# Optimization experiments

Measured on AMD Instinct MI355X. Metric: run time of the kernel, lower is better.

## Reference

```python
import jax, jax.numpy as jnp
import numpy as np

B, T, D, H = 8, 4096, 512, 512

def log_g(x):
    # log of g(x) = where(x>=0, x+0.5, sigmoid(x)) computed stably in log space
    return jnp.where(x >= 0, jnp.log(jax.nn.relu(x) + 0.5), -jax.nn.softplus(-x))

def setup_inputs() -> dict:
    key = jax.random.key(0)
    ks = jax.random.split(key, 6)
    x = jax.random.normal(ks[0], (B, T, D), dtype=jnp.float32)
    h0 = jax.random.uniform(ks[1], (B, H), dtype=jnp.float32)
    lim_z = 1.0 / np.sqrt(D)
    Wz = jax.random.uniform(ks[2], (H, D), jnp.float32, -lim_z, lim_z)
    bz = jax.random.uniform(ks[3], (H,), jnp.float32, -lim_z, lim_z)
    Wh = jax.random.uniform(ks[4], (H, D), jnp.float32, -lim_z, lim_z)
    bh = jax.random.uniform(ks[5], (H,), jnp.float32, -lim_z, lim_z)
    return {"x": x, "h0": h0, "Wz": Wz, "bz": bz, "Wh": Wh, "bh": bh}

def reference(x, h0, Wz, bz, Wh, bh):
    # gate pre-activation k: (B,T,H)
    k = jnp.einsum('btd,hd->bth', x, Wz) + bz
    log_z = -jax.nn.softplus(-k)        # log sigmoid(k)
    log_coeffs = -jax.nn.softplus(k)    # log (1 - sigmoid(k))
    log_h0 = log_g(h0)[:, None, :]      # (B,1,H)
    log_tilde_h = log_g(jnp.einsum('btd,hd->bth', x, Wh) + bh)
    # Heinsen log-space parallel scan
    log_values = jnp.concatenate([log_h0, log_z + log_tilde_h], axis=1)  # (B,T+1,H)
    a_star = jnp.pad(jnp.cumsum(log_coeffs, axis=1), ((0, 0), (1, 0), (0, 0)))  # (B,T+1,H)
    log_h = a_star + jax.lax.cumlogsumexp(log_values - a_star, axis=1)
    return jnp.exp(log_h)[:, 1:]  # (B,T,H)
```

## Files before the change

kernel.cpp:

```cpp
#include <hip/hip_runtime.h>
#include <hip/hip_fp16.h>
#include <cstdint>
#include <cstddef>

constexpr int Bb = 8, Tt = 4096, Dd = 512, Hh = 512;
constexpr int Mm = Bb * Tt;
constexpr int CHUNKS = 128;
constexpr int CLEN = Tt / CHUNKS;

typedef short short8 __attribute__((ext_vector_type(8)));
typedef float f32x4 __attribute__((ext_vector_type(4)));

#define BMT 128
#define BHT 128
#define BKT 64

__device__ inline void gload_lds16(const void* g, void* lds) {
  __builtin_amdgcn_global_load_lds(
      (const __attribute__((address_space(1))) unsigned int*)g,
      (__attribute__((address_space(3))) unsigned int*)lds,
      16, 0, 0);
}

__device__ inline unsigned short bf16_rne(float f) {
  unsigned int u = __float_as_uint(f);
  unsigned int r = (u + 0x7FFFu + ((u >> 16) & 1u)) >> 16;
  return (unsigned short)r;
}

__device__ inline uint2 pack4_bf16(const float* p) {
  uint2 hv;
  hv.x = (unsigned)bf16_rne(p[0]) | ((unsigned)bf16_rne(p[1]) << 16);
  hv.y = (unsigned)bf16_rne(p[2]) | ((unsigned)bf16_rne(p[3]) << 16);
  return hv;
}

__global__ __launch_bounds__(256) void prep_all(
    const float* __restrict__ x, const float* __restrict__ Wz,
    const float* __restrict__ Wh, unsigned short* __restrict__ xb,
    unsigned short* __restrict__ Wc) {
  int bid = blockIdx.x;
  if (bid < 16384) {
    size_t i = (size_t)bid * 256 + threadIdx.x;
    float4 w = *(const float4*)(x + i * 4);
    *(uint2*)(xb + i * 4) = pack4_bf16((const float*)&w);
  } else {
    int j = (bid - 16384) * 256 + threadIdx.x;
    const float* src = (j < 65536) ? (Wz + (size_t)j * 4)
                                   : (Wh + (size_t)(j - 65536) * 4);
    float4 w = *(const float4*)src;
    *(uint2*)(Wc + (size_t)j * 4) = pack4_bf16((const float*)&w);
  }
}

__global__ __launch_bounds__(256) void prep_w(
    const float* __restrict__ Wz, const float* __restrict__ Wh,
    unsigned short* __restrict__ Wc) {
  int j = blockIdx.x * 256 + threadIdx.x;
  const float* src = (j < 65536) ? (Wz + (size_t)j * 4)
                                 : (Wh + (size_t)(j - 65536) * 4);
  float4 w = *(const float4*)src;
  *(uint2*)(Wc + (size_t)j * 4) = pack4_bf16((const float*)&w);
}

template <int XB>
__global__ __launch_bounds__(256, 2) void gemm_fused(
    const float* __restrict__ x, const unsigned short* __restrict__ xb,
    const unsigned short* __restrict__ Wc,
    const float* __restrict__ bz, const float* __restrict__ bh,
    unsigned int* __restrict__ av,
    float* __restrict__ aggA, float* __restrict__ aggH) {
  __shared__ __align__(16) char smem[49152];
  unsigned short* Abf = (unsigned short*)smem;
  unsigned short* Bzf = (unsigned short*)(smem + 16384);
  unsigned short* Bhf = (unsigned short*)(smem + 32768);
  float* AsL = (float*)smem;
  float* HsL = (float*)(smem + 16384);

  const int tid = threadIdx.x;
  const int lane = tid & 63, wid = tid >> 6;
  int swz = (blockIdx.x & 7) * 128 + (blockIdx.x >> 3);
  const int bm = swz >> 2, hn = swz & 3;
  const int row0 = bm * BMT, h0 = hn * BHT;

  const int wr = (wid >> 1) * 64, hc = (wid & 1) * 64;
  const int fr = lane & 15, kg = lane >> 4;

  const int r8 = lane >> 3;
  const int c8 = ((lane & 7) ^ r8) * 8;
  const int fr7 = lane & 7;
  const int sk0 = (kg ^ fr7) * 8;
  const int sk1 = ((kg + 4) ^ fr7) * 8;

  f32x4 ak[4][4], ap[4][4];
#pragma unroll
  for (int i = 0; i < 4; ++i)
#pragma unroll
    for (int j = 0; j < 4; ++j) { ak[i][j] = (f32x4)0.f; ap[i][j] = (f32x4)0.f; }

  for (int k0 = 0; k0 < Dd; k0 += BKT) {
    if constexpr (XB) {
      __syncthreads();
#pragma unroll
      for (int i = 0; i < 4; ++i) {
        int rw = wid * 32 + i * 8;
        gload_lds16(xb + (size_t)(row0 + rw + r8) * Dd + k0 + c8, &Abf[rw * BKT]);
        gload_lds16(Wc + (size_t)(h0 + rw + r8) * Dd + k0 + c8, &Bzf[rw * BKT]);
        gload_lds16(Wc + (size_t)(512 + h0 + rw + r8) * Dd + k0 + c8, &Bhf[rw * BKT]);
      }
      __syncthreads();
    } else {
      float4 avx[8];
#pragma unroll
      for (int i = 0; i < 8; ++i) {
        int f = i * 256 + tid;
        avx[i] = *(const float4*)(x + (size_t)(row0 + (f >> 4)) * Dd + k0 + (f & 15) * 4);
      }
      __syncthreads();
#pragma unroll
      for (int i = 0; i < 4; ++i) {
        int rw = wid * 32 + i * 8;
        gload_lds16(Wc + (size_t)(h0 + rw + r8) * Dd + k0 + c8, &Bzf[rw * BKT]);
        gload_lds16(Wc + (size_t)(512 + h0 + rw + r8) * Dd + k0 + c8, &Bhf[rw * BKT]);
      }
#pragma unroll
      for (int i = 0; i < 8; ++i) {
        int f = i * 256 + tid;
        int r = f >> 4;
        uint2 hv = pack4_bf16((const float*)&avx[i]);
        int soff = ((((f & 15) >> 1) ^ (r & 7)) * 8) + (f & 1) * 4;
        *(uint2*)&Abf[r * BKT + soff] = hv;
      }
      __syncthreads();
    }

#pragma unroll
    for (int ks = 0; ks < 2; ++ks) {
      const int sk = ks ? sk1 : sk0;
      short8 fa[4], fz[4], fh[4];
#pragma unroll
      for (int mi = 0; mi < 4; ++mi)
        fa[mi] = *(const short8*)&Abf[(wr + mi * 16 + fr) * BKT + sk];
#pragma unroll
      for (int ni = 0; ni < 4; ++ni) {
        fz[ni] = *(const short8*)&Bzf[(hc + ni * 16 + fr) * BKT + sk];
        fh[ni] = *(const short8*)&Bhf[(hc + ni * 16 + fr) * BKT + sk];
      }
#pragma unroll
      for (int mi = 0; mi < 4; ++mi)
#pragma unroll
        for (int ni = 0; ni < 4; ++ni) {
          ak[mi][ni] = __builtin_amdgcn_mfma_f32_16x16x32_bf16(fa[mi], fz[ni], ak[mi][ni], 0, 0, 0);
          ap[mi][ni] = __builtin_amdgcn_mfma_f32_16x16x32_bf16(fa[mi], fh[ni], ap[mi][ni], 0, 0, 0);
        }
    }
  }

  __syncthreads();

#pragma unroll
  for (int ni = 0; ni < 4; ++ni) {
    int colG = h0 + hc + ni * 16 + fr;
    float bzv = bz[colG];
    float bhv = bh[colG];
#pragma unroll
    for (int mi = 0; mi < 4; ++mi) {
      float A4 = 1.f, H4 = 0.f;
#pragma unroll
      for (int j = 0; j < 4; ++j) {
        float kv = ak[mi][ni][j] + bzv;
        float pv = ap[mi][ni][j] + bhv;
        float a = 1.f / (1.f + __expf(kv));
        float z = 1.f - a;
        float g = (pv >= 0.f) ? (pv + 0.5f) : 1.f / (1.f + __expf(-pv));
        float v = z * g;
        int row = row0 + wr + mi * 16 + kg * 4 + j;
        unsigned int u = (unsigned int)__half_as_ushort(__float2half_rn(a)) |
                         ((unsigned int)__half_as_ushort(__float2half_rn(v)) << 16);
        av[(size_t)row * Hh + colG] = u;
        H4 = fmaf(a, H4, v);
        A4 *= a;
      }
      int srow = (wr >> 2) + mi * 4 + kg;
      int cl = hc + ni * 16 + fr;
      AsL[srow * BHT + cl] = A4;
      HsL[srow * BHT + cl] = H4;
    }
  }
  __syncthreads();

  const int b = row0 >> 12;
  const int cbase = (row0 & 4095) >> 5;
#pragma unroll
  for (int p0 = 0; p0 < 2; ++p0) {
    int p = p0 * 256 + tid;
    int chunk = p >> 7, cl = p & 127;
    float A = 1.f, H = 0.f;
#pragma unroll
    for (int s = 0; s < 8; ++s) {
      int srow = chunk * 8 + s;
      float As = AsL[srow * BHT + cl];
      float Hs = HsL[srow * BHT + cl];
      H = fmaf(As, H, Hs);
      A *= As;
    }
    size_t idx = ((size_t)b * CHUNKS + cbase + chunk) * Hh + h0 + cl;
    aggA[idx] = A;
    aggH[idx] = H;
  }
}

__global__ __launch_bounds__(256) void scan_carry_ks(
    const float* __restrict__ aggA, const float* __restrict__ aggH,
    const float* __restrict__ h0, float* __restrict__ carry) {
  __shared__ float As[256], Hs[256];
  const int tid = threadIdx.x;
  const int c = tid & 127;
  const int gch = blockIdx.x * 2 + (tid >> 7);
  const int b = gch >> 9, h = gch & 511;
  size_t base = (size_t)b * CHUNKS * Hh + h;
  float A = aggA[base + (size_t)c * Hh];
  float H = aggH[base + (size_t)c * Hh];
  As[tid] = A; Hs[tid] = H;
  __syncthreads();
#pragma unroll
  for (int s = 1; s < 128; s <<= 1) {
    float Al = 1.f, Hl = 0.f;
    const bool act = (c >= s);
    if (act) { Al = As[tid - s]; Hl = Hs[tid - s]; }
    __syncthreads();
    if (act) {
      H = fmaf(A, Hl, H);
      A = A * Al;
      As[tid] = A; Hs[tid] = H;
    }
    __syncthreads();
  }
  float hv = h0[(size_t)b * Hh + h];
  float g0 = (hv >= 0.f) ? (hv + 0.5f) : 1.f / (1.f + __expf(-hv));
  float cr;
  if (c == 0) cr = g0;
  else cr = fmaf(As[tid - 1], g0, Hs[tid - 1]);
  carry[base + (size_t)c * Hh] = cr;
}

__global__ __launch_bounds__(512) void scan_apply_av(
    const unsigned int* __restrict__ av, const float* __restrict__ carry,
    float* __restrict__ out) {
  const int h = threadIdx.x;
  const int bc = blockIdx.x;
  const int b = bc >> 7, c = bc & 127;
  float hp = carry[(size_t)bc * Hh + h];
  size_t base = ((size_t)b * Tt + (size_t)c * CLEN) * Hh + h;
#pragma unroll
  for (int i = 0; i < CLEN; ++i) {
    size_t idx = base + (size_t)i * Hh;
    unsigned int u = av[idx];
    float a = __half2float(__ushort_as_half((unsigned short)(u & 0xFFFFu)));
    float v = __half2float(__ushort_as_half((unsigned short)(u >> 16)));
    hp = fmaf(a, hp, v);
    out[idx] = hp;
  }
}

extern "C" void kernel_launch(void* const* d_in, const int* in_sizes, int n_in,
                              void* d_out, int out_size, void* d_ws, size_t ws_size,
                              hipStream_t stream) {
  const float* x  = (const float*)d_in[0];
  const float* h0 = (const float*)d_in[1];
  const float* Wz = (const float*)d_in[2];
  const float* bz = (const float*)d_in[3];
  const float* Wh = (const float*)d_in[4];
  const float* bh = (const float*)d_in[5];
  float* out = (float*)d_out;

  char* w = (char*)d_ws;
  unsigned int* avb    = (unsigned int*)w;
  unsigned short* Wc   = (unsigned short*)(w + 67108864);
  float* aggA          = (float*)(w + 68157440);
  float* aggH          = (float*)(w + 70254592);
  float* carry         = (float*)(w + 72351744);
  unsigned short* xb   = (unsigned short*)(w + 74448896);
  const bool useXB = ws_size >= 108003328ull;

  const int grid = (Mm / BMT) * (Hh / BHT);
  if (useXB) {
    prep_all<<<16896, 256, 0, stream>>>(x, Wz, Wh, xb, Wc);
    gemm_fused<1><<<grid, 256, 0, stream>>>(x, xb, Wc, bz, bh, avb, aggA, aggH);
  } else {
    prep_w<<<512, 256, 0, stream>>>(Wz, Wh, Wc);
    gemm_fused<0><<<grid, 256, 0, stream>>>(x, xb, Wc, bz, bh, avb, aggA, aggH);
  }
  scan_carry_ks<<<(Bb * Hh) / 2, 256, 0, stream>>>(aggA, aggH, h0, carry);
  scan_apply_av<<<Bb * CHUNKS, 512, 0, stream>>>(avb, carry, out);
}
```

Measured before the change: 106.0 us.

## Double-buffer LDS tiles and enlarge GEMM block to 256 rows with 512 threads

The fused GEMM kernel now uses 256x128 output tiles with 8 waves. In the bf16-x path it double-buffers the LDS stages, issuing the next k-tile's global-to-LDS loads before computing the current one, waited on with explicit vmcnt and raw barriers. It also raises wave priority around the MFMA section. The aim is to hide global load latency and improve operand reuse, at the cost of 128KB of LDS per block, which limits occupancy to one block per CU despite the launch bound of 2.

```diff
diff --git a/kernel.cpp b/kernel.cpp
--- a/kernel.cpp
+++ b/kernel.cpp
@@ -11,9 +11,10 @@
 typedef short short8 __attribute__((ext_vector_type(8)));
 typedef float f32x4 __attribute__((ext_vector_type(4)));
 
-#define BMT 128
+#define BMT 256
 #define BHT 128
 #define BKT 64
+#define NIT 8
 
 __device__ inline void gload_lds16(const void* g, void* lds) {
   __builtin_amdgcn_global_load_lds(
@@ -64,22 +65,21 @@
 }
 
 template <int XB>
-__global__ __launch_bounds__(256, 2) void gemm_fused(
+__global__ __launch_bounds__(512, 2) void gemm_fused(
     const float* __restrict__ x, const unsigned short* __restrict__ xb,
     const unsigned short* __restrict__ Wc,
     const float* __restrict__ bz, const float* __restrict__ bh,
     unsigned int* __restrict__ av,
     float* __restrict__ aggA, float* __restrict__ aggH) {
-  __shared__ __align__(16) char smem[49152];
-  unsigned short* Abf = (unsigned short*)smem;
-  unsigned short* Bzf = (unsigned short*)(smem + 16384);
-  unsigned short* Bhf = (unsigned short*)(smem + 32768);
+  __shared__ __align__(16) char smem[131072];
+  unsigned short* buf0 = (unsigned short*)smem;
+  unsigned short* buf1 = (unsigned short*)(smem + 65536);
   float* AsL = (float*)smem;
-  float* HsL = (float*)(smem + 16384);
+  float* HsL = (float*)(smem + 32768);
 
   const int tid = threadIdx.x;
   const int lane = tid & 63, wid = tid >> 6;
-  int swz = (blockIdx.x & 7) * 128 + (blockIdx.x >> 3);
+  int swz = (blockIdx.x & 7) * 64 + (blockIdx.x >> 3);
   const int bm = swz >> 2, hn = swz & 3;
   const int row0 = bm * BMT, h0 = hn * BHT;
 
@@ -98,53 +98,79 @@
 #pragma unroll
     for (int j = 0; j < 4; ++j) { ak[i][j] = (f32x4)0.f; ap[i][j] = (f32x4)0.f; }
 
-  for (int k0 = 0; k0 < Dd; k0 += BKT) {
+#define STAGE(T, BB)                                                           \
+  {                                                                            \
+    const int kk = (T) * BKT;                                                  \
+    unsigned short* bb = (BB);                                                 \
+    _Pragma("unroll")                                                          \
+    for (int i = 0; i < 4; ++i) {                                              \
+      int rw = wid * 32 + i * 8;                                               \
+      gload_lds16(xb + (size_t)(row0 + rw + r8) * Dd + kk + c8, bb + rw * BKT);\
+    }                                                                          \
+    _Pragma("unroll")                                                          \
+    for (int i = 0; i < 2; ++i) {                                              \
+      int rw = wid * 16 + i * 8;                                               \
+      gload_lds16(Wc + (size_t)(h0 + rw + r8) * Dd + kk + c8,                  \
+                  bb + 16384 + rw * BKT);                                      \
+      gload_lds16(Wc + (size_t)(512 + h0 + rw + r8) * Dd + kk + c8,            \
+                  bb + 24576 + rw * BKT);                                      \
+    }                                                                          \
+  }
+
+  if constexpr (XB) STAGE(0, buf0);
+
+  for (int t = 0; t < NIT; ++t) {
+    const unsigned short *Ab, *Bzb, *Bhb;
     if constexpr (XB) {
+      unsigned short* cur = (t & 1) ? buf1 : buf0;
+      unsigned short* nxt = (t & 1) ? buf0 : buf1;
+      if (t < NIT - 1) {
+        STAGE(t + 1, nxt);
+        asm volatile("s_waitcnt vmcnt(8)" ::: "memory");
+      } else {
+        asm volatile("s_waitcnt vmcnt(0)" ::: "memory");
+      }
+      __builtin_amdgcn_s_barrier();
+      Ab = cur; Bzb = cur + 16384; Bhb = cur + 24576;
+    } else {
+      const int kk = t * BKT;
+      float4 avx[8];
+#pragma unroll
+      for (int i = 0; i < 8; ++i) {
+        int f = i * 512 + tid;
+        avx[i] = *(const float4*)(x + (size_t)(row0 + (f >> 4)) * Dd + kk + (f & 15) * 4);
+      }
       __syncthreads();
 #pragma unroll
-      for (int i = 0; i < 4; ++i) {
-        int rw = wid * 32 + i * 8;
-        gload_lds16(xb + (size_t)(row0 + rw + r8) * Dd + k0 + c8, &Abf[rw * BKT]);
-        gload_lds16(Wc + (size_t)(h0 + rw + r8) * Dd + k0 + c8, &Bzf[rw * BKT]);
-        gload_lds16(Wc + (size_t)(512 + h0 + rw + r8) * Dd + k0 + c8, &Bhf[rw * BKT]);
-      }
-      __syncthreads();
-    } else {
-      float4 avx[8];
+      for (int i = 0; i < 2; ++i) {
+        int rw = wid * 16 + i * 8;
+        gload_lds16(Wc + (size_t)(h0 + rw + r8) * Dd + kk + c8, buf0 + 16384 + rw * BKT);
+        gload_lds16(Wc + (size_t)(512 + h0 + rw + r8) * Dd + kk + c8, buf0 + 24576 + rw * BKT);
+      }
 #pragma unroll
       for (int i = 0; i < 8; ++i) {
-        int f = i * 256 + tid;
-        avx[i] = *(const float4*)(x + (size_t)(row0 + (f >> 4)) * Dd + k0 + (f & 15) * 4);
-      }
-      __syncthreads();
-#pragma unroll
-      for (int i = 0; i < 4; ++i) {
-        int rw = wid * 32 + i * 8;
-        gload_lds16(Wc + (size_t)(h0 + rw + r8) * Dd + k0 + c8, &Bzf[rw * BKT]);
-        gload_lds16(Wc + (size_t)(512 + h0 + rw + r8) * Dd + k0 + c8, &Bhf[rw * BKT]);
-      }
-#pragma unroll
-      for (int i = 0; i < 8; ++i) {
-        int f = i * 256 + tid;
+        int f = i * 512 + tid;
         int r = f >> 4;
         uint2 hv = pack4_bf16((const float*)&avx[i]);
         int soff = ((((f & 15) >> 1) ^ (r & 7)) * 8) + (f & 1) * 4;
-        *(uint2*)&Abf[r * BKT + soff] = hv;
+        *(uint2*)&buf0[r * BKT + soff] = hv;
       }
       __syncthreads();
-    }
-
+      Ab = buf0; Bzb = buf0 + 16384; Bhb = buf0 + 24576;
+    }
+
+    __builtin_amdgcn_s_setprio(1);
 #pragma unroll
     for (int ks = 0; ks < 2; ++ks) {
       const int sk = ks ? sk1 : sk0;
       short8 fa[4], fz[4], fh[4];
 #pragma unroll
       for (int mi = 0; mi < 4; ++mi)
-        fa[mi] = *(const short8*)&Abf[(wr + mi * 16 + fr) * BKT + sk];
+        fa[mi] = *(const short8*)&Ab[(wr + mi * 16 + fr) * BKT + sk];
 #pragma unroll
       for (int ni = 0; ni < 4; ++ni) {
-        fz[ni] = *(const short8*)&Bzf[(hc + ni * 16 + fr) * BKT + sk];
-        fh[ni] = *(const short8*)&Bhf[(hc + ni * 16 + fr) * BKT + sk];
+        fz[ni] = *(const short8*)&Bzb[(hc + ni * 16 + fr) * BKT + sk];
+        fh[ni] = *(const short8*)&Bhb[(hc + ni * 16 + fr) * BKT + sk];
       }
 #pragma unroll
       for (int mi = 0; mi < 4; ++mi)
@@ -154,7 +180,10 @@
           ap[mi][ni] = __builtin_amdgcn_mfma_f32_16x16x32_bf16(fa[mi], fh[ni], ap[mi][ni], 0, 0, 0);
         }
     }
-  }
+    __builtin_amdgcn_s_setprio(0);
+    if constexpr (XB) __builtin_amdgcn_s_barrier();
+  }
+#undef STAGE
 
   __syncthreads();
 
@@ -163,6 +192,7 @@
     int colG = h0 + hc + ni * 16 + fr;
     float bzv = bz[colG];
     float bhv = bh[colG];
+    int cl = hc + ni * 16 + fr;
 #pragma unroll
     for (int mi = 0; mi < 4; ++mi) {
       float A4 = 1.f, H4 = 0.f;
@@ -182,7 +212,6 @@
         A4 *= a;
       }
       int srow = (wr >> 2) + mi * 4 + kg;
-      int cl = hc + ni * 16 + fr;
       AsL[srow * BHT + cl] = A4;
       HsL[srow * BHT + cl] = H4;
     }
@@ -193,7 +222,7 @@
   const int cbase = (row0 & 4095) >> 5;
 #pragma unroll
   for (int p0 = 0; p0 < 2; ++p0) {
-    int p = p0 * 256 + tid;
+    int p = p0 * 512 + tid;
     int chunk = p >> 7, cl = p & 127;
     float A = 1.f, H = 0.f;
 #pragma unroll
@@ -286,10 +315,10 @@
   const int grid = (Mm / BMT) * (Hh / BHT);
   if (useXB) {
     prep_all<<<16896, 256, 0, stream>>>(x, Wz, Wh, xb, Wc);
-    gemm_fused<1><<<grid, 256, 0, stream>>>(x, xb, Wc, bz, bh, avb, aggA, aggH);
+    gemm_fused<1><<<grid, 512, 0, stream>>>(x, xb, Wc, bz, bh, avb, aggA, aggH);
   } else {
     prep_w<<<512, 256, 0, stream>>>(Wz, Wh, Wc);
-    gemm_fused<0><<<grid, 256, 0, stream>>>(x, xb, Wc, bz, bh, avb, aggA, aggH);
+    gemm_fused<0><<<grid, 512, 0, stream>>>(x, xb, Wc, bz, bh, avb, aggA, aggH);
   }
   scan_carry_ks<<<(Bb * Hh) / 2, 256, 0, stream>>>(aggA, aggH, h0, carry);
   scan_apply_av<<<Bb * CHUNKS, 512, 0, stream>>>(avb, carry, out);
```

After: 107.9 us. Within noise of the previous version (+1.8%).

## Replace GEMM with 8-wave double-buffered pipelined kernel using 256-row tiles

Applied to the files above, without the earlier changes.

Adds a new 512-thread GEMM kernel that treats the Wz and Wh halves as a single 256-column B matrix over a 256x128 tile. It double-buffers LDS stages loaded with global_load_lds, and interleaves fragment loads with MFMA bursts under sched barriers and s_setprio. The Wh pre-activations are moved between waves through LDS as bf16 so the gate epilogue can combine them. This is meant to hide global-load latency and raise MFMA utilisation, at the cost of 128KB LDS per block and extra rounding of the Wh pre-activation to bf16.

```diff
diff --git a/kernel.cpp b/kernel.cpp
--- a/kernel.cpp
+++ b/kernel.cpp
@@ -10,10 +10,6 @@
 
 typedef short short8 __attribute__((ext_vector_type(8)));
 typedef float f32x4 __attribute__((ext_vector_type(4)));
-
-#define BMT 128
-#define BHT 128
-#define BKT 64
 
 __device__ inline void gload_lds16(const void* g, void* lds) {
   __builtin_amdgcn_global_load_lds(
@@ -27,7 +23,9 @@
   unsigned int r = (u + 0x7FFFu + ((u >> 16) & 1u)) >> 16;
   return (unsigned short)r;
 }
-
+__device__ inline float bf16_tof(unsigned short u) {
+  return __uint_as_float(((unsigned int)u) << 16);
+}
 __device__ inline uint2 pack4_bf16(const float* p) {
   uint2 hv;
   hv.x = (unsigned)bf16_rne(p[0]) | ((unsigned)bf16_rne(p[1]) << 16);
@@ -63,10 +61,223 @@
   *(uint2*)(Wc + (size_t)j * 4) = pack4_bf16((const float*)&w);
 }
 
-template <int XB>
-__global__ __launch_bounds__(256, 2) void gemm_fused(
-    const float* __restrict__ x, const unsigned short* __restrict__ xb,
-    const unsigned short* __restrict__ Wc,
+__device__ inline void gates_c(float kv, float pv, float& a, float& v) {
+  a = 1.f / (1.f + __expf(kv));
+  float z = 1.f - a;
+  float g = (pv >= 0.f) ? (pv + 0.5f) : 1.f / (1.f + __expf(-pv));
+  v = z * g;
+}
+
+#define SB() __builtin_amdgcn_sched_barrier(0)
+#define BAR() do { SB(); __builtin_amdgcn_s_barrier(); SB(); } while (0)
+
+__global__ __launch_bounds__(512, 2) void gemm8(
+    const unsigned short* __restrict__ xb, const unsigned short* __restrict__ Wc,
+    const float* __restrict__ bz, const float* __restrict__ bh,
+    unsigned int* __restrict__ av,
+    float* __restrict__ aggA, float* __restrict__ aggH) {
+  __shared__ __align__(16) char smem[131072];
+
+  const int tid = threadIdx.x;
+  const int lane = tid & 63, wid = tid >> 6;
+  const int bm = blockIdx.x >> 2, hn = blockIdx.x & 3;
+  const int row0 = bm * 256, h0 = hn * 128;
+
+  const int m = wid >> 2;
+  const int q = wid & 3;
+  const int fr = lane & 15, kg = lane >> 4, fr7 = lane & 7;
+  const int r8 = lane >> 3;
+  const int c8 = ((lane & 7) ^ r8) * 8;
+
+  f32x4 acc[8][4];
+#pragma unroll
+  for (int i = 0; i < 8; ++i)
+#pragma unroll
+    for (int j = 0; j < 4; ++j) acc[i][j] = (f32x4)0.f;
+
+#define STAGEH(T, HF)                                                          \
+  {                                                                            \
+    const int d_ = (T) & 1, kk_ = (T) * 64;                                    \
+    char* base_ = smem + d_ * 65536 + (HF) * 32768;                            \
+    _Pragma("unroll")                                                          \
+    for (int r_ = 0; r_ < 2; ++r_) {                                           \
+      int st_ = r_ * 64 + wid * 8;                                             \
+      gload_lds16(xb + (size_t)(row0 + (HF) * 128 + st_ + r8) * Dd + kk_ + c8, \
+                  base_ + st_ * 128);                                          \
+    }                                                                          \
+    _Pragma("unroll")                                                          \
+    for (int r_ = 0; r_ < 2; ++r_) {                                           \
+      int st_ = r_ * 64 + wid * 8;                                             \
+      gload_lds16(Wc + (size_t)((HF) * 512 + h0 + st_ + r8) * Dd + kk_ + c8,   \
+                  base_ + 16384 + st_ * 128);                                  \
+    }                                                                          \
+  }
+
+  STAGEH(0, 0); STAGEH(0, 1); STAGEH(1, 0);
+
+#pragma unroll
+  for (int t = 0; t < 8; ++t) {
+    if (t < 7) { asm volatile("s_waitcnt vmcnt(4)" ::: "memory"); }
+    else       { asm volatile("s_waitcnt vmcnt(0)" ::: "memory"); }
+    BAR();
+
+    const int d = t & 1;
+    const unsigned short* Ab = (const unsigned short*)(smem + d * 65536 + m * 32768);
+    const unsigned short* Bbp = (const unsigned short*)(smem + d * 65536 + (q >> 1) * 32768 + 16384);
+    const int qh = q & 1;
+
+    short8 fa[4][2], fb[4][2];
+
+#pragma unroll
+    for (int i = 0; i < 4; ++i)
+#pragma unroll
+      for (int ks = 0; ks < 2; ++ks)
+        fa[i][ks] = *(const short8*)(Ab + (i * 16 + fr) * 64 + ((kg + ks * 4) ^ fr7) * 8);
+#pragma unroll
+    for (int ni = 0; ni < 2; ++ni)
+#pragma unroll
+      for (int ks = 0; ks < 2; ++ks)
+        fb[ni][ks] = *(const short8*)(Bbp + (qh * 64 + ni * 16 + fr) * 64 + ((kg + ks * 4) ^ fr7) * 8);
+    if (t + 1 < 8) STAGEH(t + 1, 1);
+    BAR();
+    __builtin_amdgcn_s_setprio(1);
+#pragma unroll
+    for (int i = 0; i < 4; ++i)
+#pragma unroll
+      for (int j = 0; j < 2; ++j)
+#pragma unroll
+        for (int ks = 0; ks < 2; ++ks)
+          acc[i][j] = __builtin_amdgcn_mfma_f32_16x16x32_bf16(fa[i][ks], fb[j][ks], acc[i][j], 0, 0, 0);
+    __builtin_amdgcn_s_setprio(0);
+    BAR();
+
+#pragma unroll
+    for (int ni = 2; ni < 4; ++ni)
+#pragma unroll
+      for (int ks = 0; ks < 2; ++ks)
+        fb[ni][ks] = *(const short8*)(Bbp + (qh * 64 + ni * 16 + fr) * 64 + ((kg + ks * 4) ^ fr7) * 8);
+    BAR();
+    __builtin_amdgcn_s_setprio(1);
+#pragma unroll
+    for (int i = 0; i < 4; ++i)
+#pragma unroll
+      for (int j = 2; j < 4; ++j)
+#pragma unroll
+        for (int ks = 0; ks < 2; ++ks)
+          acc[i][j] = __builtin_amdgcn_mfma_f32_16x16x32_bf16(fa[i][ks], fb[j][ks], acc[i][j], 0, 0, 0);
+    __builtin_amdgcn_s_setprio(0);
+    BAR();
+
+#pragma unroll
+    for (int i = 0; i < 4; ++i)
+#pragma unroll
+      for (int ks = 0; ks < 2; ++ks)
+        fa[i][ks] = *(const short8*)(Ab + ((i + 4) * 16 + fr) * 64 + ((kg + ks * 4) ^ fr7) * 8);
+    BAR();
+    __builtin_amdgcn_s_setprio(1);
+#pragma unroll
+    for (int i = 0; i < 4; ++i)
+#pragma unroll
+      for (int j = 0; j < 2; ++j)
+#pragma unroll
+        for (int ks = 0; ks < 2; ++ks)
+          acc[i + 4][j] = __builtin_amdgcn_mfma_f32_16x16x32_bf16(fa[i][ks], fb[j][ks], acc[i + 4][j], 0, 0, 0);
+    __builtin_amdgcn_s_setprio(0);
+    BAR();
+
+    if (t + 2 < 8) STAGEH(t + 2, 0);
+    BAR();
+    __builtin_amdgcn_s_setprio(1);
+#pragma unroll
+    for (int i = 0; i < 4; ++i)
+#pragma unroll
+      for (int j = 2; j < 4; ++j)
+#pragma unroll
+        for (int ks = 0; ks < 2; ++ks)
+          acc[i + 4][j] = __builtin_amdgcn_mfma_f32_16x16x32_bf16(fa[i][ks], fb[j][ks], acc[i + 4][j], 0, 0, 0);
+    __builtin_amdgcn_s_setprio(0);
+  }
+#undef STAGEH
+
+  BAR();
+
+  if (q >= 2) {
+    char* Rb = smem + (m * 2 + (q - 2)) * 16384;
+#pragma unroll
+    for (int mi = 0; mi < 8; ++mi)
+#pragma unroll
+      for (int ni = 0; ni < 4; ++ni) {
+        int r0 = mi * 16 + kg * 4;
+        int cl = ni * 16 + fr;
+        ushort4 o;
+        o.x = bf16_rne(acc[mi][ni][0]);
+        o.y = bf16_rne(acc[mi][ni][1]);
+        o.z = bf16_rne(acc[mi][ni][2]);
+        o.w = bf16_rne(acc[mi][ni][3]);
+        *(ushort4*)(Rb + (((cl * 128 + r0) * 2) ^ ((cl & 7) << 4))) = o;
+      }
+  }
+  __syncthreads();
+
+  float* segA = (float*)(smem + 65536);
+  float* segH = (float*)(smem + 98304);
+
+  if (q < 2) {
+    const char* Rb = smem + (m * 2 + q) * 16384;
+#pragma unroll
+    for (int ni = 0; ni < 4; ++ni) {
+      int cl64 = ni * 16 + fr;
+      int cl = q * 64 + cl64;
+      int colG = h0 + cl;
+      float bzv = bz[colG], bhv = bh[colG];
+#pragma unroll
+      for (int mi = 0; mi < 8; ++mi) {
+        int r0 = mi * 16 + kg * 4;
+        ushort4 p4 = *(const ushort4*)(Rb + (((cl64 * 128 + r0) * 2) ^ ((cl64 & 7) << 4)));
+        const unsigned short* pp = (const unsigned short*)&p4;
+        float A4 = 1.f, H4 = 0.f;
+#pragma unroll
+        for (int j = 0; j < 4; ++j) {
+          float a, v;
+          gates_c(acc[mi][ni][j] + bzv, bf16_tof(pp[j]) + bhv, a, v);
+          int rowG = row0 + m * 128 + r0 + j;
+          unsigned int u = (unsigned int)__half_as_ushort(__float2half_rn(a)) |
+                           ((unsigned int)__half_as_ushort(__float2half_rn(v)) << 16);
+          av[(size_t)rowG * Hh + colG] = u;
+          H4 = fmaf(a, H4, v);
+          A4 *= a;
+        }
+        int srow = m * 32 + mi * 4 + kg;
+        segA[srow * 128 + cl] = A4;
+        segH[srow * 128 + cl] = H4;
+      }
+    }
+  }
+  __syncthreads();
+
+  const int b = row0 >> 12;
+  const int cbase = (row0 & 4095) >> 5;
+#pragma unroll
+  for (int p0i = 0; p0i < 2; ++p0i) {
+    int p = p0i * 512 + tid;
+    int ch = p >> 7, cl = p & 127;
+    float A = 1.f, H = 0.f;
+#pragma unroll
+    for (int s = 0; s < 8; ++s) {
+      int srow = ch * 8 + s;
+      float As = segA[srow * 128 + cl];
+      float Hs = segH[srow * 128 + cl];
+      H = fmaf(As, H, Hs);
+      A *= As;
+    }
+    size_t idx = ((size_t)b * CHUNKS + cbase + ch) * Hh + h0 + cl;
+    aggA[idx] = A;
+    aggH[idx] = H;
+  }
+}
+
+__global__ __launch_bounds__(256, 2) void gemm_fused_fb(
+    const float* __restrict__ x, const unsigned short* __restrict__ Wc,
     const float* __restrict__ bz, const float* __restrict__ bh,
     unsigned int* __restrict__ av,
     float* __restrict__ aggA, float* __restrict__ aggH) {
@@ -81,11 +292,9 @@
   const int lane = tid & 63, wid = tid >> 6;
   int swz = (blockIdx.x & 7) * 128 + (blockIdx.x >> 3);
   const int bm = swz >> 2, hn = swz & 3;
-  const int row0 = bm * BMT, h0 = hn * BHT;
-
+  const int row0 = bm * 128, h0 = hn * 128;
   const int wr = (wid >> 1) * 64, hc = (wid & 1) * 64;
   const int fr = lane & 15, kg = lane >> 4;
-
   const int r8 = lane >> 3;
   const int c8 = ((lane & 7) ^ r8) * 8;
   const int fr7 = lane & 7;
@@ -98,53 +307,40 @@
 #pragma unroll
     for (int j = 0; j < 4; ++j) { ak[i][j] = (f32x4)0.f; ap[i][j] = (f32x4)0.f; }
 
-  for (int k0 = 0; k0 < Dd; k0 += BKT) {
-    if constexpr (XB) {
-      __syncthreads();
-#pragma unroll
-      for (int i = 0; i < 4; ++i) {
-        int rw = wid * 32 + i * 8;
-        gload_lds16(xb + (size_t)(row0 + rw + r8) * Dd + k0 + c8, &Abf[rw * BKT]);
-        gload_lds16(Wc + (size_t)(h0 + rw + r8) * Dd + k0 + c8, &Bzf[rw * BKT]);
-        gload_lds16(Wc + (size_t)(512 + h0 + rw + r8) * Dd + k0 + c8, &Bhf[rw * BKT]);
-      }
-      __syncthreads();
-    } else {
-      float4 avx[8];
-#pragma unroll
-      for (int i = 0; i < 8; ++i) {
-        int f = i * 256 + tid;
-        avx[i] = *(const float4*)(x + (size_t)(row0 + (f >> 4)) * Dd + k0 + (f & 15) * 4);
-      }
-      __syncthreads();
-#pragma unroll
-      for (int i = 0; i < 4; ++i) {
-        int rw = wid * 32 + i * 8;
-        gload_lds16(Wc + (size_t)(h0 + rw + r8) * Dd + k0 + c8, &Bzf[rw * BKT]);
-        gload_lds16(Wc + (size_t)(512 + h0 + rw + r8) * Dd + k0 + c8, &Bhf[rw * BKT]);
-      }
-#pragma unroll
-      for (int i = 0; i < 8; ++i) {
-        int f = i * 256 + tid;
-        int r = f >> 4;
-        uint2 hv = pack4_bf16((const float*)&avx[i]);
-        int soff = ((((f & 15) >> 1) ^ (r & 7)) * 8) + (f & 1) * 4;
-        *(uint2*)&Abf[r * BKT + soff] = hv;
-      }
-      __syncthreads();
-    }
-
+  for (int k0 = 0; k0 < Dd; k0 += 64) {
+    float4 avx[8];
+#pragma unroll
+    for (int i = 0; i < 8; ++i) {
+      int f = i * 256 + tid;
+      avx[i] = *(const float4*)(x + (size_t)(row0 + (f >> 4)) * Dd + k0 + (f & 15) * 4);
+    }
+    __syncthreads();
+#pragma unroll
+    for (int i = 0; i < 4; ++i) {
+      int rw = wid * 32 + i * 8;
+      gload_lds16(Wc + (size_t)(h0 + rw + r8) * Dd + k0 + c8, &Bzf[rw * 64]);
+      gload_lds16(Wc + (size_t)(512 + h0 + rw + r8) * Dd + k0 + c8, &Bhf[rw * 64]);
+    }
+#pragma unroll
+    for (int i = 0; i < 8; ++i) {
+      int f = i * 256 + tid;
+      int r = f >> 4;
+      uint2 hv = pack4_bf16((const float*)&avx[i]);
+      int soff = ((((f & 15) >> 1) ^ (r & 7)) * 8) + (f & 1) * 4;
+      *(uint2*)&Abf[r * 64 + soff] = hv;
+    }
+    __syncthreads();
 #pragma unroll
     for (int ks = 0; ks < 2; ++ks) {
       const int sk = ks ? sk1 : sk0;
       short8 fa[4], fz[4], fh[4];
 #pragma unroll
       for (int mi = 0; mi < 4; ++mi)
-        fa[mi] = *(const short8*)&Abf[(wr + mi * 16 + fr) * BKT + sk];
+        fa[mi] = *(const short8*)&Abf[(wr + mi * 16 + fr) * 64 + sk];
 #pragma unroll
       for (int ni = 0; ni < 4; ++ni) {
-        fz[ni] = *(const short8*)&Bzf[(hc + ni * 16 + fr) * BKT + sk];
-        fh[ni] = *(const short8*)&Bhf[(hc + ni * 16 + fr) * BKT + sk];
+        fz[ni] = *(const short8*)&Bzf[(hc + ni * 16 + fr) * 64 + sk];
+        fh[ni] = *(const short8*)&Bhf[(hc + ni * 16 + fr) * 64 + sk];
       }
 #pragma unroll
       for (int mi = 0; mi < 4; ++mi)
@@ -154,26 +350,21 @@
           ap[mi][ni] = __builtin_amdgcn_mfma_f32_16x16x32_bf16(fa[mi], fh[ni], ap[mi][ni], 0, 0, 0);
         }
     }
-  }
-
-  __syncthreads();
+    __syncthreads();
+  }
 
 #pragma unroll
   for (int ni = 0; ni < 4; ++ni) {
     int colG = h0 + hc + ni * 16 + fr;
-    float bzv = bz[colG];
-    float bhv = bh[colG];
+    float bzv = bz[colG], bhv = bh[colG];
+    int cl = hc + ni * 16 + fr;
 #pragma unroll
     for (int mi = 0; mi < 4; ++mi) {
       float A4 = 1.f, H4 = 0.f;
 #pragma unroll
       for (int j = 0; j < 4; ++j) {
-        float kv = ak[mi][ni][j] + bzv;
-        float pv = ap[mi][ni][j] + bhv;
-        float a = 1.f / (1.f + __expf(kv));
-        float z = 1.f - a;
-        float g = (pv >= 0.f) ? (pv + 0.5f) : 1.f / (1.f + __expf(-pv));
-        float v = z * g;
+        float a, v;
+        gates_c(ak[mi][ni][j] + bzv, ap[mi][ni][j] + bhv, a, v);
         int row = row0 + wr + mi * 16 + kg * 4 + j;
         unsigned int u = (unsigned int)__half_as_ushort(__float2half_rn(a)) |
                          ((unsigned int)__half_as_ushort(__float2half_rn(v)) << 16);
@@ -182,29 +373,27 @@
         A4 *= a;
       }
       int srow = (wr >> 2) + mi * 4 + kg;
-      int cl = hc + ni * 16 + fr;
-      AsL[srow * BHT + cl] = A4;
-      HsL[srow * BHT + cl] = H4;
+      AsL[srow * 128 + cl] = A4;
+      HsL[srow * 128 + cl] = H4;
     }
   }
   __syncthreads();
-
   const int b = row0 >> 12;
   const int cbase = (row0 & 4095) >> 5;
 #pragma unroll
-  for (int p0 = 0; p0 < 2; ++p0) {
-    int p = p0 * 256 + tid;
-    int chunk = p >> 7, cl = p & 127;
+  for (int p0i = 0; p0i < 2; ++p0i) {
+    int p = p0i * 256 + tid;
+    int ch = p >> 7, cl = p & 127;
     float A = 1.f, H = 0.f;
 #pragma unroll
     for (int s = 0; s < 8; ++s) {
-      int srow = chunk * 8 + s;
-      float As = AsL[srow * BHT + cl];
-      float Hs = HsL[srow * BHT + cl];
+      int srow = ch * 8 + s;
+      float As = AsL[srow * 128 + cl];
+      float Hs = HsL[srow * 128 + cl];
       H = fmaf(As, H, Hs);
       A *= As;
     }
-    size_t idx = ((size_t)b * CHUNKS + cbase + chunk) * Hh + h0 + cl;
+    size_t idx = ((size_t)b * CHUNKS + cbase + ch) * Hh + h0 + cl;
     aggA[idx] = A;
     aggH[idx] = H;
   }
@@ -283,13 +472,12 @@
   unsigned short* xb   = (unsigned short*)(w + 74448896);
   const bool useXB = ws_size >= 108003328ull;
 
-  const int grid = (Mm / BMT) * (Hh / BHT);
   if (useXB) {
     prep_all<<<16896, 256, 0, stream>>>(x, Wz, Wh, xb, Wc);
-    gemm_fused<1><<<grid, 256, 0, stream>>>(x, xb, Wc, bz, bh, avb, aggA, aggH);
+    gemm8<<<(Mm / 256) * (Hh / 128), 512, 0, stream>>>(xb, Wc, bz, bh, avb, aggA, aggH);
   } else {
     prep_w<<<512, 256, 0, stream>>>(Wz, Wh, Wc);
-    gemm_fused<0><<<grid, 256, 0, stream>>>(x, xb, Wc, bz, bh, avb, aggA, aggH);
+    gemm_fused_fb<<<(Mm / 128) * (Hh / 128), 256, 0, stream>>>(x, Wc, bz, bh, avb, aggA, aggH);
   }
   scan_carry_ks<<<(Bb * Hh) / 2, 256, 0, stream>>>(aggA, aggH, h0, carry);
   scan_apply_av<<<Bb * CHUNKS, 512, 0, stream>>>(avb, carry, out);
```

After: 136.9 us. 29.1% more time.

## Fuse carry scan into apply kernel and raise GEMM occupancy hint

Applied to the files above, without the earlier changes.

Removes the separate Kogge-Stone carry-scan kernel. Each apply block now serially folds the preceding chunk aggregates to compute its own carry, which saves one launch and the carry buffer round trip. The cost is redundant work: up to 127 serial dependent loads per block, so the later chunks get long latency chains. The GEMM launch bound is also raised from 2 to 3 blocks per CU, which may force register spills.

```diff
diff --git a/kernel.cpp b/kernel.cpp
--- a/kernel.cpp
+++ b/kernel.cpp
@@ -27,7 +27,6 @@
   unsigned int r = (u + 0x7FFFu + ((u >> 16) & 1u)) >> 16;
   return (unsigned short)r;
 }
-
 __device__ inline uint2 pack4_bf16(const float* p) {
   uint2 hv;
   hv.x = (unsigned)bf16_rne(p[0]) | ((unsigned)bf16_rne(p[1]) << 16);
@@ -63,8 +62,15 @@
   *(uint2*)(Wc + (size_t)j * 4) = pack4_bf16((const float*)&w);
 }
 
+__device__ inline void gates_c(float kv, float pv, float& a, float& v) {
+  a = 1.f / (1.f + __expf(kv));
+  float z = 1.f - a;
+  float g = (pv >= 0.f) ? (pv + 0.5f) : 1.f / (1.f + __expf(-pv));
+  v = z * g;
+}
+
 template <int XB>
-__global__ __launch_bounds__(256, 2) void gemm_fused(
+__global__ __launch_bounds__(256, 3) void gemm_fused(
     const float* __restrict__ x, const unsigned short* __restrict__ xb,
     const unsigned short* __restrict__ Wc,
     const float* __restrict__ bz, const float* __restrict__ bh,
@@ -163,17 +169,14 @@
     int colG = h0 + hc + ni * 16 + fr;
     float bzv = bz[colG];
     float bhv = bh[colG];
+    int cl = hc + ni * 16 + fr;
 #pragma unroll
     for (int mi = 0; mi < 4; ++mi) {
       float A4 = 1.f, H4 = 0.f;
 #pragma unroll
       for (int j = 0; j < 4; ++j) {
-        float kv = ak[mi][ni][j] + bzv;
-        float pv = ap[mi][ni][j] + bhv;
-        float a = 1.f / (1.f + __expf(kv));
-        float z = 1.f - a;
-        float g = (pv >= 0.f) ? (pv + 0.5f) : 1.f / (1.f + __expf(-pv));
-        float v = z * g;
+        float a, v;
+        gates_c(ak[mi][ni][j] + bzv, ap[mi][ni][j] + bhv, a, v);
         int row = row0 + wr + mi * 16 + kg * 4 + j;
         unsigned int u = (unsigned int)__half_as_ushort(__float2half_rn(a)) |
                          ((unsigned int)__half_as_ushort(__float2half_rn(v)) << 16);
@@ -182,7 +185,6 @@
         A4 *= a;
       }
       int srow = (wr >> 2) + mi * 4 + kg;
-      int cl = hc + ni * 16 + fr;
       AsL[srow * BHT + cl] = A4;
       HsL[srow * BHT + cl] = H4;
     }
@@ -210,47 +212,18 @@
   }
 }
 
-__global__ __launch_bounds__(256) void scan_carry_ks(
+__global__ __launch_bounds__(512) void scan_apply_f(
     const float* __restrict__ aggA, const float* __restrict__ aggH,
-    const float* __restrict__ h0, float* __restrict__ carry) {
-  __shared__ float As[256], Hs[256];
-  const int tid = threadIdx.x;
-  const int c = tid & 127;
-  const int gch = blockIdx.x * 2 + (tid >> 7);
-  const int b = gch >> 9, h = gch & 511;
-  size_t base = (size_t)b * CHUNKS * Hh + h;
-  float A = aggA[base + (size_t)c * Hh];
-  float H = aggH[base + (size_t)c * Hh];
-  As[tid] = A; Hs[tid] = H;
-  __syncthreads();
-#pragma unroll
-  for (int s = 1; s < 128; s <<= 1) {
-    float Al = 1.f, Hl = 0.f;
-    const bool act = (c >= s);
-    if (act) { Al = As[tid - s]; Hl = Hs[tid - s]; }
-    __syncthreads();
-    if (act) {
-      H = fmaf(A, Hl, H);
-      A = A * Al;
-      As[tid] = A; Hs[tid] = H;
-    }
-    __syncthreads();
-  }
-  float hv = h0[(size_t)b * Hh + h];
-  float g0 = (hv >= 0.f) ? (hv + 0.5f) : 1.f / (1.f + __expf(-hv));
-  float cr;
-  if (c == 0) cr = g0;
-  else cr = fmaf(As[tid - 1], g0, Hs[tid - 1]);
-  carry[base + (size_t)c * Hh] = cr;
-}
-
-__global__ __launch_bounds__(512) void scan_apply_av(
-    const unsigned int* __restrict__ av, const float* __restrict__ carry,
+    const float* __restrict__ h0v, const unsigned int* __restrict__ av,
     float* __restrict__ out) {
   const int h = threadIdx.x;
   const int bc = blockIdx.x;
   const int b = bc >> 7, c = bc & 127;
-  float hp = carry[(size_t)bc * Hh + h];
+  float hv = h0v[(size_t)b * Hh + h];
+  float hp = (hv >= 0.f) ? (hv + 0.5f) : 1.f / (1.f + __expf(-hv));
+  size_t abase = (size_t)b * CHUNKS * Hh + h;
+  for (int cc = 0; cc < c; ++cc)
+    hp = fmaf(aggA[abase + (size_t)cc * Hh], hp, aggH[abase + (size_t)cc * Hh]);
   size_t base = ((size_t)b * Tt + (size_t)c * CLEN) * Hh + h;
 #pragma unroll
   for (int i = 0; i < CLEN; ++i) {
@@ -279,7 +252,6 @@
   unsigned short* Wc   = (unsigned short*)(w + 67108864);
   float* aggA          = (float*)(w + 68157440);
   float* aggH          = (float*)(w + 70254592);
-  float* carry         = (float*)(w + 72351744);
   unsigned short* xb   = (unsigned short*)(w + 74448896);
   const bool useXB = ws_size >= 108003328ull;
 
@@ -291,6 +263,5 @@
     prep_w<<<512, 256, 0, stream>>>(Wz, Wh, Wc);
     gemm_fused<0><<<grid, 256, 0, stream>>>(x, xb, Wc, bz, bh, avb, aggA, aggH);
   }
-  scan_carry_ks<<<(Bb * Hh) / 2, 256, 0, stream>>>(aggA, aggH, h0, carry);
-  scan_apply_av<<<Bb * CHUNKS, 512, 0, stream>>>(avb, carry, out);
-}
+  scan_apply_f<<<Bb * CHUNKS, 512, 0, stream>>>(aggA, aggH, h0, avb, out);
+}
```

Measured after the change: 213.8 us. 102% more time.
